# Kernel optimization log

Hardware: AMD Instinct MI355X
Metric: run time of the kernel (lower is better)

## Reference

```python
import jax, jax.numpy as jnp
import numpy as np

B, C, H1, W1 = 64, 3, 512, 512
H2, W2 = 224, 224


def setup_inputs() -> dict:
    key = jax.random.key(0)
    # images in [0,1] as produced by ToTensor / expected by ToPILImage
    x = jax.random.uniform(key, (B, C, H1, W1), dtype=jnp.float32)
    return {"input": x}


def reference(input) -> jnp.ndarray:
    # PIL Resize (default BILINEAR) performs an antialiased bilinear resize
    # when downsampling. jax.image.resize with method='bilinear' and
    # antialias=True matches this math, applied batched over [B, C].
    out_shape = (input.shape[0], input.shape[1], H2, W2)
    return jax.image.resize(input, out_shape, method="bilinear", antialias=True)
```

## Files before the change

### kernel.cpp

```cpp
#include <hip/hip_runtime.h>

#define IN_H 512
#define IN_W 512
#define OUT_H 224
#define OUT_W 224
#define OY 8
#define BLOCK 256
#define NTILE (OUT_H / OY)
#define NIMG  (64 * 3)
#define NWG   (NIMG * NTILE)


__global__ __launch_bounds__(BLOCK) void resize_aa_vfirst(
    const float* __restrict__ in, float* __restrict__ out) {

    __shared__ float s_v[OY][IN_W];
    __shared__ float s_wx[OUT_W][5];
    __shared__ int   s_ix0[OUT_W];
    __shared__ float s_wy[OY][5];
    __shared__ int   s_iy0[OY];

    int bid  = blockIdx.x;
    int wg   = (bid & 7) * (NWG / 8) + (bid >> 3);
    int img  = wg / NTILE;
    int tile = wg - img * NTILE;
    const int oy0 = tile * OY;
    const int tid = threadIdx.x;

    const float inv_scale = 16.f / 7.f;
    const float scl       = 7.f / 16.f;

    if (tid < OUT_W) {
        float cx  = (tid + 0.5f) * inv_scale - 0.5f;
        int   ix0 = (int)ceilf(cx - inv_scale);
        float w[5];
        float s = 0.f;
#pragma unroll
        for (int j = 0; j < 5; ++j) {
            int i = ix0 + j;
            float ww = 1.f - fabsf(cx - (float)i) * scl;
            ww = fmaxf(ww, 0.f);
            if (i < 0 || i >= IN_W) ww = 0.f;
            w[j] = ww;
            s += ww;
        }
        float invs = 1.f / s;
#pragma unroll
        for (int j = 0; j < 5; ++j) s_wx[tid][j] = w[j] * invs;
        s_ix0[tid] = ix0;
    } else if (tid >= 240 && tid < 240 + OY) {
        int   t   = tid - 240;
        float cy  = (oy0 + t + 0.5f) * inv_scale - 0.5f;
        int   iy0 = (int)ceilf(cy - inv_scale);
        float w[5];
        float s = 0.f;
#pragma unroll
        for (int j = 0; j < 5; ++j) {
            int i = iy0 + j;
            float ww = 1.f - fabsf(cy - (float)i) * scl;
            ww = fmaxf(ww, 0.f);
            if (i < 0 || i >= IN_H) ww = 0.f;
            w[j] = ww;
            s += ww;
        }
        float invs = 1.f / s;
#pragma unroll
        for (int j = 0; j < 5; ++j) s_wy[t][j] = w[j] * invs;
        s_iy0[t] = iy0;
    }

    __syncthreads();

    const float* src = in + (size_t)img * (IN_H * IN_W);
#pragma unroll
    for (int k = 0; k < OY * (IN_W / 4) / BLOCK; ++k) {
        int q  = tid + k * BLOCK;
        int t  = q >> 7;
        int x0 = (q & 127) << 2;
        int iy0 = s_iy0[t];
        float4 acc = make_float4(0.f, 0.f, 0.f, 0.f);
#pragma unroll
        for (int j = 0; j < 5; ++j) {
            float ww = s_wy[t][j];
            int r = min(max(iy0 + j, 0), IN_H - 1);
            float4 v = *(const float4*)(src + (size_t)r * IN_W + x0);
            acc.x = fmaf(ww, v.x, acc.x);
            acc.y = fmaf(ww, v.y, acc.y);
            acc.z = fmaf(ww, v.z, acc.z);
            acc.w = fmaf(ww, v.w, acc.w);
        }
        *(float4*)(&s_v[t][x0]) = acc;
    }

    __syncthreads();

    for (int idx = tid; idx < OY * OUT_W; idx += BLOCK) {
        int t  = idx / OUT_W;
        int ox = idx - t * OUT_W;
        int ix0 = s_ix0[ox];
        float acc = 0.f;
#pragma unroll
        for (int j = 0; j < 5; ++j) {
            int c = min(max(ix0 + j, 0), IN_W - 1);
            acc = fmaf(s_wx[ox][j], s_v[t][c], acc);
        }
        out[((size_t)img * OUT_H + (oy0 + t)) * OUT_W + ox] = acc;
    }
}

extern "C" void kernel_launch(void* const* d_in, const int* in_sizes, int n_in,
                              void* d_out, int out_size, void* d_ws, size_t ws_size,
                              hipStream_t stream) {
    const float* in = (const float*)d_in[0];
    float* out = (float*)d_out;
    dim3 block(BLOCK);
    dim3 grid(NWG);
    hipLaunchKernelGGL(resize_aa_vfirst, grid, block, 0, stream, in, out);
}
```

Measured before the change: 284.1 us.

## Assign one output row per wavefront and drop the second block barrier

Each 64-lane wavefront now computes one output row end to end. It builds its vertical weights in registers, accumulates the vertical pass for a full 512-wide row into its own LDS slice, then does the horizontal pass from that slice. Tiles shrink from 8 to 4 rows, so the grid doubles and the block-wide barrier between the two passes goes away. The trade-off is that overlapping input rows are shared across fewer output rows per block, which leans more on L2 for reuse.

```diff
diff --git a/kernel.cpp b/kernel.cpp
--- a/kernel.cpp
+++ b/kernel.cpp
@@ -4,28 +4,29 @@
 #define IN_W 512
 #define OUT_H 224
 #define OUT_W 224
-#define OY 8
 #define BLOCK 256
-#define NTILE (OUT_H / OY)
+#define OYB 4
+#define NTILE (OUT_H / OYB)
 #define NIMG  (64 * 3)
 #define NWG   (NIMG * NTILE)
 
 
-__global__ __launch_bounds__(BLOCK) void resize_aa_vfirst(
+__global__ __launch_bounds__(BLOCK) void resize_aa_wave(
     const float* __restrict__ in, float* __restrict__ out) {
 
-    __shared__ float s_v[OY][IN_W];
+    __shared__ float s_v[OYB][IN_W];
     __shared__ float s_wx[OUT_W][5];
     __shared__ int   s_ix0[OUT_W];
-    __shared__ float s_wy[OY][5];
-    __shared__ int   s_iy0[OY];
+
+    const int tid  = threadIdx.x;
+    const int wave = tid >> 6;
+    const int lane = tid & 63;
 
     int bid  = blockIdx.x;
     int wg   = (bid & 7) * (NWG / 8) + (bid >> 3);
     int img  = wg / NTILE;
     int tile = wg - img * NTILE;
-    const int oy0 = tile * OY;
-    const int tid = threadIdx.x;
+    const int oy = tile * OYB + wave;
 
     const float inv_scale = 16.f / 7.f;
     const float scl       = 7.f / 16.f;
@@ -48,63 +49,59 @@
 #pragma unroll
         for (int j = 0; j < 5; ++j) s_wx[tid][j] = w[j] * invs;
         s_ix0[tid] = ix0;
-    } else if (tid >= 240 && tid < 240 + OY) {
-        int   t   = tid - 240;
-        float cy  = (oy0 + t + 0.5f) * inv_scale - 0.5f;
-        int   iy0 = (int)ceilf(cy - inv_scale);
-        float w[5];
-        float s = 0.f;
-#pragma unroll
-        for (int j = 0; j < 5; ++j) {
-            int i = iy0 + j;
-            float ww = 1.f - fabsf(cy - (float)i) * scl;
-            ww = fmaxf(ww, 0.f);
-            if (i < 0 || i >= IN_H) ww = 0.f;
-            w[j] = ww;
-            s += ww;
-        }
-        float invs = 1.f / s;
-#pragma unroll
-        for (int j = 0; j < 5; ++j) s_wy[t][j] = w[j] * invs;
-        s_iy0[t] = iy0;
     }
-
     __syncthreads();
 
+    float cy  = (oy + 0.5f) * inv_scale - 0.5f;
+    int   iy0 = (int)ceilf(cy - inv_scale);
+    float wy[5];
+    int   ry[5];
+    float sy = 0.f;
+#pragma unroll
+    for (int j = 0; j < 5; ++j) {
+        int i = iy0 + j;
+        float ww = 1.f - fabsf(cy - (float)i) * scl;
+        ww = fmaxf(ww, 0.f);
+        if (i < 0 || i >= IN_H) ww = 0.f;
+        wy[j] = ww;
+        sy += ww;
+        ry[j] = min(max(i, 0), IN_H - 1);
+    }
+    float invsy = 1.f / sy;
+#pragma unroll
+    for (int j = 0; j < 5; ++j) wy[j] *= invsy;
+
     const float* src = in + (size_t)img * (IN_H * IN_W);
+    float4 a0 = make_float4(0.f, 0.f, 0.f, 0.f);
+    float4 a1 = make_float4(0.f, 0.f, 0.f, 0.f);
 #pragma unroll
-    for (int k = 0; k < OY * (IN_W / 4) / BLOCK; ++k) {
-        int q  = tid + k * BLOCK;
-        int t  = q >> 7;
-        int x0 = (q & 127) << 2;
-        int iy0 = s_iy0[t];
-        float4 acc = make_float4(0.f, 0.f, 0.f, 0.f);
+    for (int j = 0; j < 5; ++j) {
+        const float* rp = src + (size_t)ry[j] * IN_W;
+        float4 v0 = *(const float4*)(rp + 4 * lane);
+        float4 v1 = *(const float4*)(rp + 256 + 4 * lane);
+        float  w  = wy[j];
+        a0.x = fmaf(w, v0.x, a0.x); a0.y = fmaf(w, v0.y, a0.y);
+        a0.z = fmaf(w, v0.z, a0.z); a0.w = fmaf(w, v0.w, a0.w);
+        a1.x = fmaf(w, v1.x, a1.x); a1.y = fmaf(w, v1.y, a1.y);
+        a1.z = fmaf(w, v1.z, a1.z); a1.w = fmaf(w, v1.w, a1.w);
+    }
+    *(float4*)(&s_v[wave][4 * lane])       = a0;
+    *(float4*)(&s_v[wave][256 + 4 * lane]) = a1;
+
+    float* orow = out + ((size_t)img * OUT_H + oy) * OUT_W;
 #pragma unroll
-        for (int j = 0; j < 5; ++j) {
-            float ww = s_wy[t][j];
-            int r = min(max(iy0 + j, 0), IN_H - 1);
-            float4 v = *(const float4*)(src + (size_t)r * IN_W + x0);
-            acc.x = fmaf(ww, v.x, acc.x);
-            acc.y = fmaf(ww, v.y, acc.y);
-            acc.z = fmaf(ww, v.z, acc.z);
-            acc.w = fmaf(ww, v.w, acc.w);
+    for (int i = 0; i < 4; ++i) {
+        int ox = i * 64 + lane;
+        if (i < 3 || ox < OUT_W) {
+            int ix0 = s_ix0[ox];
+            float acc = 0.f;
+#pragma unroll
+            for (int j = 0; j < 5; ++j) {
+                int c = min(max(ix0 + j, 0), IN_W - 1);
+                acc = fmaf(s_wx[ox][j], s_v[wave][c], acc);
+            }
+            orow[ox] = acc;
         }
-        *(float4*)(&s_v[t][x0]) = acc;
-    }
-
-    __syncthreads();
-
-    for (int idx = tid; idx < OY * OUT_W; idx += BLOCK) {
-        int t  = idx / OUT_W;
-        int ox = idx - t * OUT_W;
-        int ix0 = s_ix0[ox];
-        float acc = 0.f;
-#pragma unroll
-        for (int j = 0; j < 5; ++j) {
-            int c = min(max(ix0 + j, 0), IN_W - 1);
-            acc = fmaf(s_wx[ox][j], s_v[t][c], acc);
-        }
-        out[((size_t)img * OUT_H + (oy0 + t)) * OUT_W + ox] = acc;
     }
 }
 
@@ -115,5 +112,5 @@
     float* out = (float*)d_out;
     dim3 block(BLOCK);
     dim3 grid(NWG);
-    hipLaunchKernelGGL(resize_aa_vfirst, grid, block, 0, stream, in, out);
+    hipLaunchKernelGGL(resize_aa_wave, grid, block, 0, stream, in, out);
 }
```

Result: no change. 280.0 us (-1.4%).
